# Kernel tuning notes

Measured on AMD Instinct MI355X. Metric: run time of the kernel, lower is better.

The kernel has to match this reference:

```python
import jax, jax.numpy as jnp
import numpy as np

N_NODES = 50000
N_EDGES = 640000
IN_CH = 128
HID_CH = 256


def setup_inputs() -> dict:
    key = jax.random.key(0)
    k_x, k_e, k_wl, k_bl, k_wr = jax.random.split(key, 5)
    x = jax.random.normal(k_x, (N_NODES, IN_CH), dtype=jnp.float32)
    edge_index = jax.random.randint(k_e, (2, N_EDGES), 0, N_NODES, dtype=jnp.int64)
    # PyG SAGEConv params: lin_l (applied to aggregated neighbors, with bias),
    # lin_r (root/self weight, no bias). Glorot-ish init scale.
    s = 1.0 / np.sqrt(IN_CH)
    W_l = jax.random.uniform(k_wl, (IN_CH, HID_CH), jnp.float32, -s, s)
    b_l = jnp.zeros((HID_CH,), dtype=jnp.float32)
    W_r = jax.random.uniform(k_wr, (IN_CH, HID_CH), jnp.float32, -s, s)
    return {"x": x, "edge_index": edge_index, "W_l": W_l, "b_l": b_l, "W_r": W_r}


def reference(x, edge_index, W_l, b_l, W_r):
    src, dst = edge_index[0], edge_index[1]
    # Gather source-node features per edge and mean-aggregate onto targets.
    msgs = x[src]                                            # [E, in]
    agg = jax.ops.segment_sum(msgs, dst, num_segments=N_NODES)   # [N, in]
    cnt = jax.ops.segment_sum(jnp.ones((N_EDGES,), x.dtype), dst,
                              num_segments=N_NODES)          # [N]
    mean = agg / jnp.maximum(cnt, 1.0)[:, None]
    # out = lin_l(mean_neighbors) + lin_r(x)
    return mean @ W_l + b_l + x @ W_r
```

## Files before the change

kernel.cpp:

```cpp
#include <hip/hip_runtime.h>


constexpr int N_NODES = 50000;
constexpr int N_EDGES = 640000;
constexpr int GEMM_TILES = (N_NODES + 127) / 128;
constexpr int CAP = 64;

constexpr int SCAT_BLOCKS  = N_EDGES / 1024;
constexpr int PREPX_BLOCKS = N_NODES * 32 / 256;
constexpr int WPREP_BLOCKS = 256;

typedef __attribute__((ext_vector_type(8))) short short8;
typedef __attribute__((ext_vector_type(4))) float f32x4;
typedef __attribute__((ext_vector_type(2))) float f32x2;
typedef _Float16 half8 __attribute__((ext_vector_type(8)));

__device__ inline unsigned short f2h(float f) {
    _Float16 h = (_Float16)f;
    return __builtin_bit_cast(unsigned short, h);
}

__global__ __launch_bounds__(256) void prep_k(const float* __restrict__ x,
                                              const int* __restrict__ ei,
                                              const float* __restrict__ Wl,
                                              const float* __restrict__ Wr,
                                              unsigned int* __restrict__ Abf_u,
                                              unsigned short* __restrict__ Wimg,
                                              int* __restrict__ cnt,
                                              int* __restrict__ slots,
                                              unsigned int* __restrict__ Xf8_u) {
    int bid = blockIdx.x, tid = threadIdx.x;
    if (bid < SCAT_BLOCKS) {
        int base = bid * 1024 + tid;
#pragma unroll
        for (int k = 0; k < 4; k++) {
            int e   = base + k * 256;
            int src = ei[e];
            int dst = ei[N_EDGES + e];
            int pos = atomicAdd(&cnt[dst], 1);
            if (pos < CAP) slots[(size_t)dst * CAP + pos] = src;
        }
    } else if (bid < SCAT_BLOCKS + PREPX_BLOCKS) {
        int t = (bid - SCAT_BLOCKS) * 256 + tid;
        float4 v = reinterpret_cast<const float4*>(x)[t];
        unsigned int p0 = (unsigned int)f2h(v.x) | ((unsigned int)f2h(v.y) << 16);
        unsigned int p1 = (unsigned int)f2h(v.z) | ((unsigned int)f2h(v.w) << 16);
        int row = t >> 5, c = t & 31;
        reinterpret_cast<uint2*>(Abf_u)[(size_t)row * 64 + 32 + c] =
            make_uint2(p0, p1);
        int u8 = __builtin_amdgcn_cvt_pk_fp8_f32(v.x, v.y, 0, false);
        u8     = __builtin_amdgcn_cvt_pk_fp8_f32(v.z, v.w, u8, true);
        Xf8_u[t] = (unsigned int)u8;
    } else {
        int t = (bid - SCAT_BLOCKS - PREPX_BLOCKS) * 256 + tid;
        int k = t >> 8, n = t & 255;
        float v = (k < 128) ? Wl[k * 256 + n] : Wr[(k - 128) * 256 + n];
        Wimg[(size_t)(k >> 5) * 8192 + n * 32 + (k & 31)] = f2h(v);
    }
}

__global__ __launch_bounds__(256) void agg_k(const int* __restrict__ cnt,
                                             const int* __restrict__ slots,
                                             const unsigned int* __restrict__ Xf8_u,
                                             unsigned int* __restrict__ Abf_u) {
    int wave = (blockIdx.x * 256 + threadIdx.x) >> 6;
    int lane = threadIdx.x & 63;
    int g    = lane >> 3;
    int sub  = lane & 7;
    int node = wave * 8 + g;
    if (node >= N_NODES) return;
    int dc   = cnt[node];
    int deg  = (dc > CAP) ? CAP : dc;
    const int* sl = slots + (size_t)node * CAP;
    const uint4* X8 = reinterpret_cast<const uint4*>(Xf8_u);

    f32x2 a0 = {0.f, 0.f}, a1 = {0.f, 0.f}, a2 = {0.f, 0.f}, a3 = {0.f, 0.f};
    f32x2 a4 = {0.f, 0.f}, a5 = {0.f, 0.f}, a6 = {0.f, 0.f}, a7 = {0.f, 0.f};

#define LOADV(vj, J)                                                    \
    uint4 vj = make_uint4(0, 0, 0, 0);                                  \
    {                                                                   \
        int sj = __shfl(slv, (J), 8);                                   \
        if (base + (J) < deg)                                           \
            vj = X8[(size_t)sj * 8 + sub];                              \
    }
#define ACCV(vj)                                                              \
    {                                                                         \
        a0 += __builtin_amdgcn_cvt_pk_f32_fp8(vj.x, false);                   \
        a1 += __builtin_amdgcn_cvt_pk_f32_fp8(vj.x, true);                    \
        a2 += __builtin_amdgcn_cvt_pk_f32_fp8(vj.y, false);                   \
        a3 += __builtin_amdgcn_cvt_pk_f32_fp8(vj.y, true);                    \
        a4 += __builtin_amdgcn_cvt_pk_f32_fp8(vj.z, false);                   \
        a5 += __builtin_amdgcn_cvt_pk_f32_fp8(vj.z, true);                    \
        a6 += __builtin_amdgcn_cvt_pk_f32_fp8(vj.w, false);                   \
        a7 += __builtin_amdgcn_cvt_pk_f32_fp8(vj.w, true);                    \
    }

    for (int base = 0; base < deg; base += 8) {
        int slv = sl[base + sub];
        LOADV(v0, 0) LOADV(v1, 1) LOADV(v2, 2) LOADV(v3, 3)
        LOADV(v4, 4) LOADV(v5, 5) LOADV(v6, 6) LOADV(v7, 7)
        ACCV(v0) ACCV(v1) ACCV(v2) ACCV(v3)
        ACCV(v4) ACCV(v5) ACCV(v6) ACCV(v7)
    }
#undef LOADV
#undef ACCV

    float inv = (dc > 0) ? 1.0f / (float)dc : 0.0f;
    uint4 o0, o1;
    o0.x = (unsigned int)f2h(a0.x * inv) | ((unsigned int)f2h(a0.y * inv) << 16);
    o0.y = (unsigned int)f2h(a1.x * inv) | ((unsigned int)f2h(a1.y * inv) << 16);
    o0.z = (unsigned int)f2h(a2.x * inv) | ((unsigned int)f2h(a2.y * inv) << 16);
    o0.w = (unsigned int)f2h(a3.x * inv) | ((unsigned int)f2h(a3.y * inv) << 16);
    o1.x = (unsigned int)f2h(a4.x * inv) | ((unsigned int)f2h(a4.y * inv) << 16);
    o1.y = (unsigned int)f2h(a5.x * inv) | ((unsigned int)f2h(a5.y * inv) << 16);
    o1.z = (unsigned int)f2h(a6.x * inv) | ((unsigned int)f2h(a6.y * inv) << 16);
    o1.w = (unsigned int)f2h(a7.x * inv) | ((unsigned int)f2h(a7.y * inv) << 16);
    uint4* A4 = reinterpret_cast<uint4*>(Abf_u);
    A4[(size_t)node * 32 + sub * 2]     = o0;
    A4[(size_t)node * 32 + sub * 2 + 1] = o1;
}

__global__ __launch_bounds__(512) void gemm_k(const unsigned short* __restrict__ Abf,
                                              const unsigned short* __restrict__ Wimg,
                                              const float* __restrict__ bl,
                                              float* __restrict__ out) {
    __shared__ unsigned short As[128 * 40];
    __shared__ unsigned short Bs[256 * 40];

    int tid  = threadIdx.x;
    int w8   = tid >> 6;
    int wm   = w8 >> 2;
    int wn   = w8 & 3;
    int lane = tid & 63;
    int m15  = lane & 15;
    int quad = lane >> 4;
    int bm   = blockIdx.x * 128;

    f32x4 zero4 = {0.f, 0.f, 0.f, 0.f};
    f32x4 acc[4][4];
#pragma unroll
    for (int rt = 0; rt < 4; rt++)
#pragma unroll
        for (int ct = 0; ct < 4; ct++) acc[rt][ct] = zero4;

    for (int kc = 0; kc < 8; kc++) {
        {
            int row = tid >> 2, q = tid & 3;
            int grow = bm + row;
            short8 v = {0, 0, 0, 0, 0, 0, 0, 0};
            if (grow < N_NODES)
                v = *reinterpret_cast<const short8*>(
                        Abf + (size_t)grow * 256 + kc * 32 + q * 8);
            *reinterpret_cast<short8*>(As + row * 40 + q * 8) = v;
        }
        {
            int n = tid >> 1, half = tid & 1;
            const unsigned short* src =
                Wimg + (size_t)kc * 8192 + n * 32 + half * 16;
            unsigned short* dstp = Bs + n * 40 + half * 16;
#pragma unroll
            for (int s = 0; s < 2; s++) {
                short8 v = *reinterpret_cast<const short8*>(src + s * 8);
                *reinterpret_cast<short8*>(dstp + s * 8) = v;
            }
        }
        __syncthreads();

        half8 Af[4], Bf[4];
#pragma unroll
        for (int rt = 0; rt < 4; rt++)
            Af[rt] = *reinterpret_cast<const half8*>(
                         As + (wm * 64 + rt * 16 + m15) * 40 + quad * 8);
#pragma unroll
        for (int ct = 0; ct < 4; ct++)
            Bf[ct] = *reinterpret_cast<const half8*>(
                         Bs + (wn * 64 + ct * 16 + m15) * 40 + quad * 8);
#pragma unroll
        for (int rt = 0; rt < 4; rt++)
#pragma unroll
            for (int ct = 0; ct < 4; ct++)
                acc[rt][ct] = __builtin_amdgcn_mfma_f32_16x16x32_f16(
                    Af[rt], Bf[ct], acc[rt][ct], 0, 0, 0);
        __syncthreads();
    }

    float bias[4];
#pragma unroll
    for (int ct = 0; ct < 4; ct++) bias[ct] = bl[wn * 64 + ct * 16 + m15];
#pragma unroll
    for (int rt = 0; rt < 4; rt++) {
        int rb = bm + wm * 64 + rt * 16 + quad * 4;
#pragma unroll
        for (int r = 0; r < 4; r++) {
            int row = rb + r;
            if (row < N_NODES) {
#pragma unroll
                for (int ct = 0; ct < 4; ct++)
                    out[(size_t)row * 256 + wn * 64 + ct * 16 + m15] =
                        acc[rt][ct][r] + bias[ct];
            }
        }
    }
}

extern "C" void kernel_launch(void* const* d_in, const int* in_sizes, int n_in,
                              void* d_out, int out_size, void* d_ws, size_t ws_size,
                              hipStream_t stream) {
    const float* x  = (const float*)d_in[0];
    const int*   ei = (const int*)d_in[1];
    const float* Wl = (const float*)d_in[2];
    const float* bl = (const float*)d_in[3];
    const float* Wr = (const float*)d_in[4];
    float* out = (float*)d_out;

    unsigned short* Abf  = (unsigned short*)d_ws;
    unsigned short* Wimg = Abf + (size_t)N_NODES * 256;
    int* cnt   = (int*)(Wimg + 65536);
    int* slots = cnt + N_NODES;
    unsigned int* Xf8 = (unsigned int*)(slots + (size_t)N_NODES * CAP);

    hipMemsetAsync(cnt, 0, N_NODES * sizeof(int), stream);

    prep_k<<<SCAT_BLOCKS + PREPX_BLOCKS + WPREP_BLOCKS, 256, 0, stream>>>(
        x, ei, Wl, Wr, (unsigned int*)Abf, Wimg, cnt, slots, Xf8);
    agg_k<<<(N_NODES / 8 * 64 + 255) / 256, 256, 0, stream>>>(
        cnt, slots, Xf8, (unsigned int*)Abf);
    gemm_k<<<GEMM_TILES, 512, 0, stream>>>(Abf, Wimg, bl, out);
}
```

Measured before the change: 155.3 us.

## Drop LDS staging in GEMM, use register double-buffered global fragment loads

The GEMM kernel no longer stages A and W tiles through shared memory with two barriers per k-chunk. Each wave now loads its MFMA fragments straight from global memory into registers, double-buffered, so the next chunk's loads overlap the current chunk's MFMAs. The tile shrinks to 64 rows per 256-thread block, which doubles the grid. The cost is less coalesced, redundant global reads of W and A across waves, which rely on L2 hits. The last tile also reads past N_NODES rows into the adjacent workspace; those results are masked on store.

```diff
diff --git a/kernel.cpp b/kernel.cpp
--- a/kernel.cpp
+++ b/kernel.cpp
@@ -3,7 +3,7 @@
 
 constexpr int N_NODES = 50000;
 constexpr int N_EDGES = 640000;
-constexpr int GEMM_TILES = (N_NODES + 127) / 128;
+constexpr int GEMM_TILES = (N_NODES + 63) / 64;
 constexpr int CAP = 64;
 
 constexpr int SCAT_BLOCKS  = N_EDGES / 1024;
@@ -121,21 +121,16 @@
     A4[(size_t)node * 32 + sub * 2 + 1] = o1;
 }
 
-__global__ __launch_bounds__(512) void gemm_k(const unsigned short* __restrict__ Abf,
+__global__ __launch_bounds__(256) void gemm_k(const unsigned short* __restrict__ Abf,
                                               const unsigned short* __restrict__ Wimg,
                                               const float* __restrict__ bl,
                                               float* __restrict__ out) {
-    __shared__ unsigned short As[128 * 40];
-    __shared__ unsigned short Bs[256 * 40];
-
     int tid  = threadIdx.x;
-    int w8   = tid >> 6;
-    int wm   = w8 >> 2;
-    int wn   = w8 & 3;
+    int w    = tid >> 6;
     int lane = tid & 63;
     int m15  = lane & 15;
     int quad = lane >> 4;
-    int bm   = blockIdx.x * 128;
+    int bm   = blockIdx.x * 64;
 
     f32x4 zero4 = {0.f, 0.f, 0.f, 0.f};
     f32x4 acc[4][4];
@@ -144,60 +139,68 @@
 #pragma unroll
         for (int ct = 0; ct < 4; ct++) acc[rt][ct] = zero4;
 
+    const unsigned short* Abase = Abf + ((size_t)(bm + m15) * 256 + quad * 8);
+    const unsigned short* Bbase =
+        Wimg + ((size_t)(w * 64 + m15) * 32 + quad * 8);
+
+    half8 Af0[4], Bf0[4], Af1[4], Bf1[4];
+#pragma unroll
+    for (int rt = 0; rt < 4; rt++)
+        Af0[rt] = *reinterpret_cast<const half8*>(Abase + rt * 4096);
+#pragma unroll
+    for (int ct = 0; ct < 4; ct++)
+        Bf0[ct] = *reinterpret_cast<const half8*>(Bbase + ct * 512);
+
+#pragma unroll
     for (int kc = 0; kc < 8; kc++) {
-        {
-            int row = tid >> 2, q = tid & 3;
-            int grow = bm + row;
-            short8 v = {0, 0, 0, 0, 0, 0, 0, 0};
-            if (grow < N_NODES)
-                v = *reinterpret_cast<const short8*>(
-                        Abf + (size_t)grow * 256 + kc * 32 + q * 8);
-            *reinterpret_cast<short8*>(As + row * 40 + q * 8) = v;
+        if (kc & 1) {
+            if (kc < 7) {
+#pragma unroll
+                for (int rt = 0; rt < 4; rt++)
+                    Af0[rt] = *reinterpret_cast<const half8*>(
+                        Abase + (kc + 1) * 32 + rt * 4096);
+#pragma unroll
+                for (int ct = 0; ct < 4; ct++)
+                    Bf0[ct] = *reinterpret_cast<const half8*>(
+                        Bbase + (size_t)(kc + 1) * 8192 + ct * 512);
+            }
+#pragma unroll
+            for (int rt = 0; rt < 4; rt++)
+#pragma unroll
+                for (int ct = 0; ct < 4; ct++)
+                    acc[rt][ct] = __builtin_amdgcn_mfma_f32_16x16x32_f16(
+                        Af1[rt], Bf1[ct], acc[rt][ct], 0, 0, 0);
+        } else {
+#pragma unroll
+            for (int rt = 0; rt < 4; rt++)
+                Af1[rt] = *reinterpret_cast<const half8*>(
+                    Abase + (kc + 1) * 32 + rt * 4096);
+#pragma unroll
+            for (int ct = 0; ct < 4; ct++)
+                Bf1[ct] = *reinterpret_cast<const half8*>(
+                    Bbase + (size_t)(kc + 1) * 8192 + ct * 512);
+#pragma unroll
+            for (int rt = 0; rt < 4; rt++)
+#pragma unroll
+                for (int ct = 0; ct < 4; ct++)
+                    acc[rt][ct] = __builtin_amdgcn_mfma_f32_16x16x32_f16(
+                        Af0[rt], Bf0[ct], acc[rt][ct], 0, 0, 0);
         }
-        {
-            int n = tid >> 1, half = tid & 1;
-            const unsigned short* src =
-                Wimg + (size_t)kc * 8192 + n * 32 + half * 16;
-            unsigned short* dstp = Bs + n * 40 + half * 16;
-#pragma unroll
-            for (int s = 0; s < 2; s++) {
-                short8 v = *reinterpret_cast<const short8*>(src + s * 8);
-                *reinterpret_cast<short8*>(dstp + s * 8) = v;
-            }
-        }
-        __syncthreads();
-
-        half8 Af[4], Bf[4];
-#pragma unroll
-        for (int rt = 0; rt < 4; rt++)
-            Af[rt] = *reinterpret_cast<const half8*>(
-                         As + (wm * 64 + rt * 16 + m15) * 40 + quad * 8);
-#pragma unroll
-        for (int ct = 0; ct < 4; ct++)
-            Bf[ct] = *reinterpret_cast<const half8*>(
-                         Bs + (wn * 64 + ct * 16 + m15) * 40 + quad * 8);
-#pragma unroll
-        for (int rt = 0; rt < 4; rt++)
-#pragma unroll
-            for (int ct = 0; ct < 4; ct++)
-                acc[rt][ct] = __builtin_amdgcn_mfma_f32_16x16x32_f16(
-                    Af[rt], Bf[ct], acc[rt][ct], 0, 0, 0);
-        __syncthreads();
     }
 
     float bias[4];
 #pragma unroll
-    for (int ct = 0; ct < 4; ct++) bias[ct] = bl[wn * 64 + ct * 16 + m15];
+    for (int ct = 0; ct < 4; ct++) bias[ct] = bl[w * 64 + ct * 16 + m15];
 #pragma unroll
     for (int rt = 0; rt < 4; rt++) {
-        int rb = bm + wm * 64 + rt * 16 + quad * 4;
+        int rb = bm + rt * 16 + quad * 4;
 #pragma unroll
         for (int r = 0; r < 4; r++) {
             int row = rb + r;
             if (row < N_NODES) {
 #pragma unroll
                 for (int ct = 0; ct < 4; ct++)
-                    out[(size_t)row * 256 + wn * 64 + ct * 16 + m15] =
+                    out[(size_t)row * 256 + w * 64 + ct * 16 + m15] =
                         acc[rt][ct][r] + bias[ct];
             }
         }
@@ -226,5 +229,5 @@
         x, ei, Wl, Wr, (unsigned int*)Abf, Wimg, cnt, slots, Xf8);
     agg_k<<<(N_NODES / 8 * 64 + 255) / 256, 256, 0, stream>>>(
         cnt, slots, Xf8, (unsigned int*)Abf);
-    gemm_k<<<GEMM_TILES, 512, 0, stream>>>(Abf, Wimg, bl, out);
-}
+    gemm_k<<<GEMM_TILES, 256, 0, stream>>>(Abf, Wimg, bl, out);
+}
```

After: 168.7 us. +8.6%, slower.
